# Optimization experiments

Measured on AMD Instinct MI355X. Metric: run time of the kernel, lower is better.

## Reference

```python
import jax, jax.numpy as jnp
import numpy as np

T, B, Y, X, C = 9, 2, 128, 128, 64
W = (T - 1) // 2
WIN, HEADS = 8, 4
EPS = 1e-3  # keras LayerNormalization default epsilon


def _get_indices(center, size):
    right = list(range(center, size, 2))
    left = list(range(center - 2, -1, -2))
    idx = np.array(left[::-1] + right, dtype=np.int32)
    return np.clip(idx, 1, size - 2)


def _pyramid_indices(t):
    levels = []
    size, center = t, (t - 1) // 2
    while size > 1:
        c = _get_indices(center, size)
        levels.append((c - 1, c, c + 1))
        center = int(np.where(c == center)[0][0])
        size = len(c)
    return levels


LEVELS = _pyramid_indices(T)            # 3 levels for T=9: sizes 5, 3, 1
CIN = [C * (l + 1) for l in range(len(LEVELS))]    # 64, 128, 192
COUT = [C * (l + 2) for l in range(len(LEVELS))]   # 128, 192, 256


def _window_attention(q, kv, wqkv, bqkv, wo, bo):
    # WindowSpatialAttention: non-overlapping WINxWIN windows, MHA of q over kv.
    N, Yd, Xd, Cd = q.shape
    w, h = WIN, HEADS
    dh = Cd // h
    nY, nX = Yd // w, Xd // w

    def to_win(t):
        t = t.reshape(N, nY, w, nX, w, Cd).transpose(0, 1, 3, 2, 4, 5)
        return t.reshape(N * nY * nX, w * w, Cd)

    qw, kvw = to_win(q), to_win(kv)
    qp = (qw @ wqkv[0] + bqkv[0]).reshape(-1, w * w, h, dh)
    kp = (kvw @ wqkv[1] + bqkv[1]).reshape(-1, w * w, h, dh)
    vp = (kvw @ wqkv[2] + bqkv[2]).reshape(-1, w * w, h, dh)
    logits = jnp.einsum('nqhd,nkhd->nhqk', qp, kp) / jnp.sqrt(jnp.float32(dh))
    attn = jax.nn.softmax(logits, axis=-1)
    out = jnp.einsum('nhqk,nkhd->nqhd', attn, vp).reshape(-1, w * w, Cd)
    out = out @ wo + bo
    out = out.reshape(N, nY, nX, w, w, Cd).transpose(0, 1, 3, 2, 4, 5)
    return out.reshape(N, Yd, Xd, Cd)


def _forward(x, params):
    fidx = np.arange(T) - W  # relative frame indices, static (non frame-aware)
    current = x
    level1 = None
    for l, (pi, ci, ni) in enumerate(LEVELS):
        emb, lng, lnb, wqkv, bqkv, wo, bo, cw, cb = params[l]
        cin = current.shape[-1]
        # additive relative temporal embedding, indexed by frame offset + W
        t_emb = emb[fidx + W]                       # [Tl, cin]
        cur = current + t_emb[:, None, None, None, :]
        mu = cur.mean(-1, keepdims=True)
        var = cur.var(-1, keepdims=True)
        cur = (cur - mu) * jax.lax.rsqrt(var + EPS) * lng + lnb
        S = len(ci)
        prev = cur[pi].reshape(S * B, Y, X, cin)
        cen = cur[ci].reshape(S * B, Y, X, cin)
        nxt = cur[ni].reshape(S * B, Y, X, cin)
        q = jnp.concatenate([cen, prev, cen, nxt], axis=0)
        kv = jnp.concatenate([prev, cen, nxt, cen], axis=0)
        att = _window_attention(q, kv, wqkv, bqkv, wo, bo)
        parts = jnp.split(att, 4, axis=0)           # SplitBatch(n_splits=4)
        comb = jnp.concatenate(parts, axis=-1)      # Combine: concat + 1x1 conv
        down = jax.nn.relu(comb @ cw + cb)
        if S > 1:
            down = down.reshape(S, B, Y, X, down.shape[-1])
        if l == 0:
            level1 = down
        current = down
        fidx = fidx[ci]
    return current, level1


def setup_inputs() -> dict:
    key = jax.random.key(0)
    ks = iter(jax.random.split(key, 64))
    inp = {'x': jax.random.normal(next(ks), (T, B, Y, X, C), jnp.float32)}
    for l, (ci, co) in enumerate(zip(CIN, COUT)):
        inp[f'emb{l}'] = 0.02 * jax.random.normal(next(ks), (T, ci), jnp.float32)
        inp[f'lng{l}'] = jnp.ones((ci,), jnp.float32)
        inp[f'lnb{l}'] = jnp.zeros((ci,), jnp.float32)
        inp[f'wqkv{l}'] = 0.02 * jax.random.normal(next(ks), (3, ci, ci), jnp.float32)
        inp[f'bqkv{l}'] = jnp.zeros((3, ci), jnp.float32)
        inp[f'wo{l}'] = 0.02 * jax.random.normal(next(ks), (ci, ci), jnp.float32)
        inp[f'bo{l}'] = jnp.zeros((ci,), jnp.float32)
        inp[f'cw{l}'] = 0.02 * jax.random.normal(next(ks), (4 * ci, co), jnp.float32)
        inp[f'cb{l}'] = jnp.zeros((co,), jnp.float32)
    return inp


def reference(x, emb0, lng0, lnb0, wqkv0, bqkv0, wo0, bo0, cw0, cb0,
              emb1, lng1, lnb1, wqkv1, bqkv1, wo1, bo1, cw1, cb1,
              emb2, lng2, lnb2, wqkv2, bqkv2, wo2, bo2, cw2, cb2):
    params = [
        (emb0, lng0, lnb0, wqkv0, bqkv0, wo0, bo0, cw0, cb0),
        (emb1, lng1, lnb1, wqkv1, bqkv1, wo1, bo1, cw1, cb1),
        (emb2, lng2, lnb2, wqkv2, bqkv2, wo2, bo2, cw2, cb2),
    ]
    return _forward(x, params)
```

## Files before the change

kernel.cpp:

```cpp
#include <hip/hip_runtime.h>

typedef _Float16 f16;
typedef f16 f16x4 __attribute__((ext_vector_type(4)));
typedef f16 f16x8 __attribute__((ext_vector_type(8)));
typedef float f32x4 __attribute__((ext_vector_type(4)));

#define MFMA16(a, b, c) __builtin_amdgcn_mfma_f32_16x16x16f16((a), (b), (c), 0, 0, 0)
#define MFMA32(a, b, c) __builtin_amdgcn_mfma_f32_16x16x32_f16((a), (b), (c), 0, 0, 0)

struct Meta   { int pi[5], ci[5], ni[5]; };
struct EmbMap { int m[9]; };

template <int CIN>
__global__ __launch_bounds__(256) void ln_kernel(
    const float* in, long lda, const float* __restrict__ emb,
    const float* __restrict__ lng, const float* __restrict__ lnb,
    f16* out, long ldo, EmbMap em) {
  long row = (long)blockIdx.x * 4 + (threadIdx.x >> 6);
  int t = (int)(row >> 15);
  int lane = threadIdx.x & 63;
  constexpr int NCH = CIN / 64;
  const float* xr = in + row * lda;
  const float* er = emb + (long)em.m[t] * CIN;
  float v[NCH];
  float s = 0.f;
#pragma unroll
  for (int i = 0; i < NCH; ++i) { int c = lane + (i << 6); v[i] = xr[c] + er[c]; s += v[i]; }
#pragma unroll
  for (int o = 32; o >= 1; o >>= 1) s += __shfl_xor(s, o);
  float mu = s * (1.f / CIN), ss = 0.f;
#pragma unroll
  for (int i = 0; i < NCH; ++i) { float d = v[i] - mu; ss += d * d; }
#pragma unroll
  for (int o = 32; o >= 1; o >>= 1) ss += __shfl_xor(ss, o);
  float inv = rsqrtf(ss * (1.f / CIN) + 1e-3f);
  f16* orow = out + row * ldo;
#pragma unroll
  for (int i = 0; i < NCH; ++i) {
    int c = lane + (i << 6);
    orow[c] = (f16)((v[i] - mu) * inv * lng[c] + lnb[c]);
  }
}

template <int CIN>
__global__ __launch_bounds__(64) void wT_kernel(const float* __restrict__ wqkv,
                                                f16* __restrict__ wqkvT) {
  int j = blockIdx.x;
  int which = j / CIN, jj = j % CIN;
  const float* src = wqkv + (long)which * CIN * CIN + jj;
  f16* dst = wqkvT + (long)j * CIN;
  for (int c = threadIdx.x; c < CIN; c += 64) dst[c] = (f16)src[(long)c * CIN];
}

template <int CIN, int CO>
__global__ __launch_bounds__(256) void woc_kernel(
    const float* __restrict__ wo, const float* __restrict__ bo,
    const float* __restrict__ cw, const float* __restrict__ cb,
    f16* __restrict__ wocT, float* __restrict__ fb) {
  __shared__ float scw[4 * CIN];
  __shared__ float red[256];
  int o = blockIdx.x;
  for (int i = threadIdx.x; i < 4 * CIN; i += 256) scw[i] = cw[(long)i * CO + o];
  __syncthreads();
  for (int pm = threadIdx.x; pm < 4 * CIN; pm += 256) {
    int p = pm / CIN, mm = pm % CIN;
    const float* wr = wo + (long)mm * CIN;
    const float* sc = scw + p * CIN;
    float s = 0.f;
    for (int c = 0; c < CIN; ++c) s += wr[c] * sc[c];
    wocT[(long)o * 4 * CIN + pm] = (f16)s;
  }
  float part = 0.f;
  for (int i = threadIdx.x; i < 4 * CIN; i += 256) part += bo[i % CIN] * scw[i];
  red[threadIdx.x] = part;
  __syncthreads();
  for (int st = 128; st > 0; st >>= 1) {
    if (threadIdx.x < st) red[threadIdx.x] += red[threadIdx.x + st];
    __syncthreads();
  }
  if (threadIdx.x == 0) fb[o] = cb[o] + red[0];
}

template <int CIN>
__global__ __launch_bounds__(256) void proj_kernel(
    const f16* __restrict__ cur, long lda, const f16* __restrict__ wT,
    const float* __restrict__ bqkv, f16* __restrict__ gq, f16* __restrict__ gk,
    f16* __restrict__ gvt) {
  constexpr int KS = CIN / 32;
  constexpr int NT = CIN / 16;
  constexpr int C8 = CIN / 8;
  __shared__ f16 sB[CIN * CIN];
  int which = blockIdx.x;
  long win = blockIdx.y;
  long img = win >> 8;
  int wid = (int)(win & 255);
  int wy = wid >> 4, wx = wid & 15;
  int w = threadIdx.x >> 6, lane = threadIdx.x & 63;
  int r16 = lane & 15, kq = lane >> 4;

  int tok = w * 16 + r16;
  long orig = img * 16384 + (long)(wy * 8 + (tok >> 3)) * 128 + wx * 8 + (tok & 7);
  const f16* arow = cur + orig * lda + kq * 8;
  f16x8 a[KS];
#pragma unroll
  for (int ks = 0; ks < KS; ++ks) a[ks] = *(const f16x8*)(arow + ks * 32);

  const f16* wsrc = wT + (long)which * CIN * CIN;
  for (int idx = threadIdx.x; idx < CIN * C8; idx += 256) {
    int j = idx / C8, c8 = idx % C8;
    f16x8 v = *(const f16x8*)(wsrc + idx * 8);
    int off = ((j * CIN + c8 * 8) * 2) ^ ((j & 7) << 4);
    *(f16x8*)((char*)sB + off) = v;
  }
  __syncthreads();

  f32x4 acc[NT] = {};
#pragma unroll
  for (int ks = 0; ks < KS; ++ks) {
#pragma unroll
    for (int t = 0; t < NT; ++t) {
      int off = (((t * 16 + r16) * CIN + ks * 32 + kq * 8) * 2) ^ ((r16 & 7) << 4);
      f16x8 bb = *(const f16x8*)((char*)sB + off);
      acc[t] = MFMA32(a[ks], bb, acc[t]);
    }
  }
  __syncthreads();

  if (which < 2) {
#pragma unroll
    for (int t = 0; t < NT; ++t) {
      float bias = bqkv[which * CIN + t * 16 + r16];
#pragma unroll
      for (int rg = 0; rg < 4; ++rg) {
        int r = w * 16 + kq * 4 + rg;
        int c = t * 16 + r16;
        int off = ((r * CIN + c) * 2) ^ ((r & 7) << 4);
        *(f16*)((char*)sB + off) = (f16)(acc[t][rg] + bias);
      }
    }
    __syncthreads();
    f16* dst = (which ? gk : gq) + win * 64 * CIN;
    for (int idx = threadIdx.x; idx < 64 * C8; idx += 256) {
      int r = idx / C8, c8 = idx % C8;
      int off = ((r * CIN + c8 * 8) * 2) ^ ((r & 7) << 4);
      f16x8 v = *(const f16x8*)((char*)sB + off);
      *(f16x8*)(dst + r * CIN + c8 * 8) = v;
    }
  } else {
#pragma unroll
    for (int t = 0; t < NT; ++t) {
      float bias = bqkv[2 * CIN + t * 16 + r16];
#pragma unroll
      for (int rg = 0; rg < 4; ++rg) {
        int c = t * 16 + r16;
        int pos = w * 16 + kq * 4 + rg;
        int off = ((c * 64 + pos) * 2) ^ ((c & 7) << 4);
        *(f16*)((char*)sB + off) = (f16)(acc[t][rg] + bias);
      }
    }
    __syncthreads();
    for (int c = threadIdx.x; c < CIN; c += 256) {
      f16* dst = gvt + (win * CIN + c) * 64;
#pragma unroll
      for (int p8 = 0; p8 < 8; ++p8) {
        int off = ((c * 64 + p8 * 8) * 2) ^ ((c & 7) << 4);
        *(f16x8*)(dst + p8 * 8) = *(const f16x8*)((char*)sB + off);
      }
    }
  }
}

template <int CIN, int DH, int CO>
__global__ __launch_bounds__(256) void attn_kernel(
    const f16* __restrict__ gq, const f16* __restrict__ gk,
    const f16* __restrict__ gvt, const f16* __restrict__ wocT,
    const float* __restrict__ fb, float* __restrict__ out, Meta m) {
  constexpr int NKS = DH / 16;
  constexpr int CO4 = CO / 4;
  constexpr int NTC = CO4 / 16;
  constexpr int NKD = CIN / 16;
  constexpr float scale = (DH == 16) ? 0.25f : (DH == 32) ? 0.1767766952966369f
                                                          : 0.1443375672974064f;
  __shared__ f16 O[64 * CIN];

  int img = blockIdx.y;
  int sidx = img >> 1, b = img & 1;
  int wid = blockIdx.x;
  int wy = wid >> 4, wx = wid & 15;
  int h = threadIdx.x >> 6, lane = threadIdx.x & 63;
  int r16 = lane & 15, kq = lane >> 4;
  int fpi = m.pi[sidx], fci = m.ci[sidx], fni = m.ni[sidx];

  f32x4 dn[NTC][4] = {};

  for (int p = 0; p < 4; ++p) {
    int qfr = (p == 1) ? fpi : ((p == 3) ? fni : fci);
    int kfr = (p == 0) ? fpi : ((p == 2) ? fni : fci);
    long qwin = (long)((qfr * 2 + b) * 256 + wid);
    long kwin = (long)((kfr * 2 + b) * 256 + wid);

    f16x4 kf[4][NKS];
#pragma unroll
    for (int tj = 0; tj < 4; ++tj)
#pragma unroll
      for (int ks = 0; ks < NKS; ++ks)
        kf[tj][ks] = *(const f16x4*)(gk + (kwin * 64 + tj * 16 + r16) * CIN +
                                     h * DH + ks * 16 + kq * 4);
    f32x4 sc[4][4] = {};
#pragma unroll
    for (int ti = 0; ti < 4; ++ti) {
      f16x4 qf[NKS];
#pragma unroll
      for (int ks = 0; ks < NKS; ++ks)
        qf[ks] = *(const f16x4*)(gq + (qwin * 64 + ti * 16 + r16) * CIN +
                                 h * DH + ks * 16 + kq * 4);
#pragma unroll
      for (int tj = 0; tj < 4; ++tj)
#pragma unroll
        for (int ks = 0; ks < NKS; ++ks)
          sc[tj][ti] = MFMA16(kf[tj][ks], qf[ks], sc[tj][ti]);
    }

    f16x4 pa[4][4];
#pragma unroll
    for (int ti = 0; ti < 4; ++ti) {
      float mx = -1e30f;
#pragma unroll
      for (int tj = 0; tj < 4; ++tj)
#pragma unroll
        for (int rg = 0; rg < 4; ++rg) mx = fmaxf(mx, sc[tj][ti][rg]);
      mx = fmaxf(mx, __shfl_xor(mx, 16));
      mx = fmaxf(mx, __shfl_xor(mx, 32));
      float sum = 0.f;
#pragma unroll
      for (int tj = 0; tj < 4; ++tj)
#pragma unroll
        for (int rg = 0; rg < 4; ++rg) {
          float e = __expf((sc[tj][ti][rg] - mx) * scale);
          sc[tj][ti][rg] = e;
          sum += e;
        }
      sum += __shfl_xor(sum, 16);
      sum += __shfl_xor(sum, 32);
      float inv = 1.f / sum;
#pragma unroll
      for (int tj = 0; tj < 4; ++tj) {
        f16x4 pv;
#pragma unroll
        for (int rg = 0; rg < 4; ++rg) pv[rg] = (f16)(sc[tj][ti][rg] * inv);
        pa[tj][ti] = pv;
      }
    }

#pragma unroll
    for (int dt = 0; dt < NKS; ++dt) {
      f16x4 va[4];
#pragma unroll
      for (int jt = 0; jt < 4; ++jt)
        va[jt] = *(const f16x4*)(gvt + (kwin * CIN + h * DH + dt * 16 + r16) * 64 +
                                 jt * 16 + kq * 4);
#pragma unroll
      for (int ti = 0; ti < 4; ++ti) {
        f32x4 po = {};
#pragma unroll
        for (int jt = 0; jt < 4; ++jt) po = MFMA16(va[jt], pa[jt][ti], po);
        int i = ti * 16 + r16;
        int c0 = h * DH + dt * 16 + kq * 4;
        f16x4 pk;
#pragma unroll
        for (int rg = 0; rg < 4; ++rg) pk[rg] = (f16)po[rg];
        int off = ((i * CIN + c0) * 2) ^ ((i & 7) << 4);
        *(f16x4*)((char*)O + off) = pk;
      }
    }
    __syncthreads();

#pragma unroll
    for (int ck = 0; ck < NKD; ++ck) {
      f16x4 ob[4];
#pragma unroll
      for (int ti = 0; ti < 4; ++ti) {
        int i = ti * 16 + r16;
        int off = ((i * CIN + ck * 16 + kq * 4) * 2) ^ ((i & 7) << 4);
        ob[ti] = *(const f16x4*)((char*)O + off);
      }
#pragma unroll
      for (int ot = 0; ot < NTC; ++ot) {
        f16x4 wa = *(const f16x4*)(wocT + ((long)(h * CO4 + ot * 16 + r16)) * 4 * CIN +
                                   p * CIN + ck * 16 + kq * 4);
#pragma unroll
        for (int ti = 0; ti < 4; ++ti) dn[ot][ti] = MFMA16(wa, ob[ti], dn[ot][ti]);
      }
    }
    __syncthreads();
  }

#pragma unroll
  for (int ot = 0; ot < NTC; ++ot) {
    f32x4 fb4 = *(const f32x4*)(fb + h * CO4 + ot * 16 + kq * 4);
#pragma unroll
    for (int ti = 0; ti < 4; ++ti) {
      int i = ti * 16 + r16;
      long gtok = (long)img * 16384 + (wy * 8 + (i >> 3)) * 128 + wx * 8 + (i & 7);
      f32x4 v;
#pragma unroll
      for (int rg = 0; rg < 4; ++rg) v[rg] = fmaxf(dn[ot][ti][rg] + fb4[rg], 0.f);
      *(f32x4*)(out + gtok * CO + h * CO4 + ot * 16 + kq * 4) = v;
    }
  }
}

extern "C" void kernel_launch(void* const* d_in, const int* in_sizes, int n_in,
                              void* d_out, int out_size, void* d_ws, size_t ws_size,
                              hipStream_t stream) {
  const float* x = (const float*)d_in[0];
#define PRM(l, k) ((const float*)d_in[1 + 9 * (l) + (k)])
  float* outCur = (float*)d_out;
  float* outL1 = (float*)d_out + 8388608;

  char* ws = (char*)d_ws;
  const size_t OFF_B = 125829120ull;
  const size_t OFF_W = OFF_B + 75497472ull;
  f16* qkvbase = (f16*)ws;
  char* wsB = ws + OFF_B;
  float* accum1 = (float*)wsB;
  f16* wqkvT = (f16*)(ws + OFF_W);
  f16* wocT = (f16*)(ws + OFF_W + 262144);
  float* fb = (float*)(ws + OFF_W + 262144 + 524288);

  Meta m0 = {{0, 1, 3, 5, 6}, {1, 2, 4, 6, 7}, {2, 3, 5, 7, 8}};
  Meta m1 = {{0, 1, 2, 0, 0}, {1, 2, 3, 0, 0}, {2, 3, 4, 0, 0}};
  Meta m2 = {{0, 0, 0, 0, 0}, {1, 0, 0, 0, 0}, {2, 0, 0, 0, 0}};
  EmbMap em0 = {{0, 1, 2, 3, 4, 5, 6, 7, 8}};
  EmbMap em1 = {{1, 2, 4, 6, 7, 0, 0, 0, 0}};
  EmbMap em2 = {{2, 4, 6, 0, 0, 0, 0, 0, 0}};

  {
    constexpr int CIN = 64, DH = 16, CO = 128, TL = 9, S = 5;
    long ntok = (long)TL * 2 * 16384;
    f16 *gq = qkvbase, *gk = gq + ntok * CIN, *gvt = gk + ntok * CIN;
    f16* cur = (f16*)wsB;
    ln_kernel<CIN><<<dim3((unsigned)(ntok / 4)), 256, 0, stream>>>(
        x, CIN, PRM(0, 0), PRM(0, 1), PRM(0, 2), cur, CIN, em0);
    wT_kernel<CIN><<<dim3(3 * CIN), 64, 0, stream>>>(PRM(0, 3), wqkvT);
    woc_kernel<CIN, CO><<<dim3(CO), 256, 0, stream>>>(PRM(0, 5), PRM(0, 6), PRM(0, 7), PRM(0, 8), wocT, fb);
    proj_kernel<CIN><<<dim3(3, (unsigned)(ntok / 64)), 256, 0, stream>>>(
        cur, CIN, wqkvT, PRM(0, 4), gq, gk, gvt);
    attn_kernel<CIN, DH, CO><<<dim3(256, S * 2), 256, 0, stream>>>(
        gq, gk, gvt, wocT, fb, outL1, m0);
  }
  {
    constexpr int CIN = 128, DH = 32, CO = 192, TL = 5, S = 3;
    long ntok = (long)TL * 2 * 16384;
    f16 *gq = qkvbase, *gk = gq + ntok * CIN, *gvt = gk + ntok * CIN;
    f16* cur = (f16*)wsB;
    ln_kernel<CIN><<<dim3((unsigned)(ntok / 4)), 256, 0, stream>>>(
        outL1, CIN, PRM(1, 0), PRM(1, 1), PRM(1, 2), cur, CIN, em1);
    wT_kernel<CIN><<<dim3(3 * CIN), 64, 0, stream>>>(PRM(1, 3), wqkvT);
    woc_kernel<CIN, CO><<<dim3(CO), 256, 0, stream>>>(PRM(1, 5), PRM(1, 6), PRM(1, 7), PRM(1, 8), wocT, fb);
    proj_kernel<CIN><<<dim3(3, (unsigned)(ntok / 64)), 256, 0, stream>>>(
        cur, CIN, wqkvT, PRM(1, 4), gq, gk, gvt);
    attn_kernel<CIN, DH, CO><<<dim3(256, S * 2), 256, 0, stream>>>(
        gq, gk, gvt, wocT, fb, accum1, m1);
  }
  {
    constexpr int CIN = 192, DH = 48, CO = 256, TL = 3, S = 1;
    long ntok = (long)TL * 2 * 16384;
    f16 *gq = qkvbase, *gk = gq + ntok * CIN, *gvt = gk + ntok * CIN;
    f16* cur = (f16*)accum1;
    ln_kernel<CIN><<<dim3((unsigned)(ntok / 4)), 256, 0, stream>>>(
        accum1, CIN, PRM(2, 0), PRM(2, 1), PRM(2, 2), cur, 384, em2);
    wT_kernel<CIN><<<dim3(3 * CIN), 64, 0, stream>>>(PRM(2, 3), wqkvT);
    woc_kernel<CIN, CO><<<dim3(CO), 256, 0, stream>>>(PRM(2, 5), PRM(2, 6), PRM(2, 7), PRM(2, 8), wocT, fb);
    proj_kernel<CIN><<<dim3(3, (unsigned)(ntok / 64)), 256, 0, stream>>>(
        cur, 384, wqkvT, PRM(2, 4), gq, gk, gvt);
    attn_kernel<CIN, DH, CO><<<dim3(256, S * 2), 256, 0, stream>>>(
        gq, gk, gvt, wocT, fb, outCur, m2);
  }
#undef PRM
}
```

Before: 690.8 us.

## Use 16x16x32 MFMA, drop softmax max pass, double-buffer attention LDS tile

The attention kernel now uses the 16x16x32 f16 MFMA for the QK^T product and for the fused output/conv projection. To feed it, the fused projection weights are repacked into an 8-element interleaved layout. Softmax drops the row-max subtraction and computes exp2 with a pre-folded log2e scale. V fragments are loaded before the score computation, and the shared O tile is double-buffered so one __syncthreads per pass can be removed. Skipping the max subtraction risks overflow if logits become large, and the fully unrolled pass loop may increase register pressure.

```diff
diff --git a/kernel.cpp b/kernel.cpp
--- a/kernel.cpp
+++ b/kernel.cpp
@@ -56,7 +56,7 @@
 __global__ __launch_bounds__(256) void woc_kernel(
     const float* __restrict__ wo, const float* __restrict__ bo,
     const float* __restrict__ cw, const float* __restrict__ cb,
-    f16* __restrict__ wocT, float* __restrict__ fb) {
+    f16* __restrict__ wocA, float* __restrict__ fb) {
   __shared__ float scw[4 * CIN];
   __shared__ float red[256];
   int o = blockIdx.x;
@@ -68,7 +68,7 @@
     const float* sc = scw + p * CIN;
     float s = 0.f;
     for (int c = 0; c < CIN; ++c) s += wr[c] * sc[c];
-    wocT[(long)o * 4 * CIN + pm] = (f16)s;
+    wocA[((long)(pm >> 3) * CO + o) * 8 + (pm & 7)] = (f16)s;
   }
   float part = 0.f;
   for (int i = threadIdx.x; i < 4 * CIN; i += 256) part += bo[i % CIN] * scw[i];
@@ -173,15 +173,18 @@
 template <int CIN, int DH, int CO>
 __global__ __launch_bounds__(256) void attn_kernel(
     const f16* __restrict__ gq, const f16* __restrict__ gk,
-    const f16* __restrict__ gvt, const f16* __restrict__ wocT,
+    const f16* __restrict__ gvt, const f16* __restrict__ wocA,
     const float* __restrict__ fb, float* __restrict__ out, Meta m) {
   constexpr int NKS = DH / 16;
+  constexpr int NK8 = DH / 32;
+  constexpr int NK4 = (DH % 32) / 16;
   constexpr int CO4 = CO / 4;
   constexpr int NTC = CO4 / 16;
-  constexpr int NKD = CIN / 16;
+  constexpr int NKD = CIN / 32;
   constexpr float scale = (DH == 16) ? 0.25f : (DH == 32) ? 0.1767766952966369f
                                                           : 0.1443375672974064f;
-  __shared__ f16 O[64 * CIN];
+  constexpr float escale = scale * 1.4426950408889634f;
+  __shared__ f16 O[2][64 * CIN];
 
   int img = blockIdx.y;
   int sidx = img >> 1, b = img & 1;
@@ -193,51 +196,66 @@
 
   f32x4 dn[NTC][4] = {};
 
+#pragma unroll
   for (int p = 0; p < 4; ++p) {
     int qfr = (p == 1) ? fpi : ((p == 3) ? fni : fci);
     int kfr = (p == 0) ? fpi : ((p == 2) ? fni : fci);
     long qwin = (long)((qfr * 2 + b) * 256 + wid);
     long kwin = (long)((kfr * 2 + b) * 256 + wid);
 
-    f16x4 kf[4][NKS];
-#pragma unroll
-    for (int tj = 0; tj < 4; ++tj)
-#pragma unroll
-      for (int ks = 0; ks < NKS; ++ks)
-        kf[tj][ks] = *(const f16x4*)(gk + (kwin * 64 + tj * 16 + r16) * CIN +
-                                     h * DH + ks * 16 + kq * 4);
-    f32x4 sc[4][4] = {};
+    f16x8 kf8[4][NK8 ? NK8 : 1];
+    f16x4 kf4[4][NK4 ? NK4 : 1];
+#pragma unroll
+    for (int tj = 0; tj < 4; ++tj) {
+      const f16* kb = gk + (kwin * 64 + tj * 16 + r16) * CIN + h * DH;
+      if constexpr (NK8 > 0)
+#pragma unroll
+        for (int n = 0; n < NK8; ++n)
+          kf8[tj][n] = *(const f16x8*)(kb + n * 32 + kq * 8);
+      if constexpr (NK4 > 0)
+#pragma unroll
+        for (int n = 0; n < NK4; ++n)
+          kf4[tj][n] = *(const f16x4*)(kb + NK8 * 32 + n * 16 + kq * 4);
+    }
+    f16x4 va[NKS][4];
+#pragma unroll
+    for (int dt = 0; dt < NKS; ++dt)
+#pragma unroll
+      for (int jt = 0; jt < 4; ++jt)
+        va[dt][jt] = *(const f16x4*)(gvt + (kwin * CIN + h * DH + dt * 16 + r16) * 64 +
+                                     jt * 16 + kq * 4);
+
+    f16x4 pa[4][4];
 #pragma unroll
     for (int ti = 0; ti < 4; ++ti) {
-      f16x4 qf[NKS];
-#pragma unroll
-      for (int ks = 0; ks < NKS; ++ks)
-        qf[ks] = *(const f16x4*)(gq + (qwin * 64 + ti * 16 + r16) * CIN +
-                                 h * DH + ks * 16 + kq * 4);
+      const f16* qb = gq + (qwin * 64 + ti * 16 + r16) * CIN + h * DH;
+      f32x4 s4[4] = {};
+      if constexpr (NK8 > 0) {
+        f16x8 qf8[NK8];
+#pragma unroll
+        for (int n = 0; n < NK8; ++n) qf8[n] = *(const f16x8*)(qb + n * 32 + kq * 8);
+#pragma unroll
+        for (int tj = 0; tj < 4; ++tj)
+#pragma unroll
+          for (int n = 0; n < NK8; ++n) s4[tj] = MFMA32(kf8[tj][n], qf8[n], s4[tj]);
+      }
+      if constexpr (NK4 > 0) {
+        f16x4 qf4[NK4];
+#pragma unroll
+        for (int n = 0; n < NK4; ++n)
+          qf4[n] = *(const f16x4*)(qb + NK8 * 32 + n * 16 + kq * 4);
+#pragma unroll
+        for (int tj = 0; tj < 4; ++tj)
+#pragma unroll
+          for (int n = 0; n < NK4; ++n) s4[tj] = MFMA16(kf4[tj][n], qf4[n], s4[tj]);
+      }
+      float sum = 0.f;
 #pragma unroll
       for (int tj = 0; tj < 4; ++tj)
 #pragma unroll
-        for (int ks = 0; ks < NKS; ++ks)
-          sc[tj][ti] = MFMA16(kf[tj][ks], qf[ks], sc[tj][ti]);
-    }
-
-    f16x4 pa[4][4];
-#pragma unroll
-    for (int ti = 0; ti < 4; ++ti) {
-      float mx = -1e30f;
-#pragma unroll
-      for (int tj = 0; tj < 4; ++tj)
-#pragma unroll
-        for (int rg = 0; rg < 4; ++rg) mx = fmaxf(mx, sc[tj][ti][rg]);
-      mx = fmaxf(mx, __shfl_xor(mx, 16));
-      mx = fmaxf(mx, __shfl_xor(mx, 32));
-      float sum = 0.f;
-#pragma unroll
-      for (int tj = 0; tj < 4; ++tj)
-#pragma unroll
         for (int rg = 0; rg < 4; ++rg) {
-          float e = __expf((sc[tj][ti][rg] - mx) * scale);
-          sc[tj][ti][rg] = e;
+          float e = __builtin_amdgcn_exp2f(s4[tj][rg] * escale);
+          s4[tj][rg] = e;
           sum += e;
         }
       sum += __shfl_xor(sum, 16);
@@ -247,52 +265,47 @@
       for (int tj = 0; tj < 4; ++tj) {
         f16x4 pv;
 #pragma unroll
-        for (int rg = 0; rg < 4; ++rg) pv[rg] = (f16)(sc[tj][ti][rg] * inv);
+        for (int rg = 0; rg < 4; ++rg) pv[rg] = (f16)(s4[tj][rg] * inv);
         pa[tj][ti] = pv;
       }
     }
 
+    char* Ob = (char*)O[p & 1];
 #pragma unroll
     for (int dt = 0; dt < NKS; ++dt) {
-      f16x4 va[4];
-#pragma unroll
-      for (int jt = 0; jt < 4; ++jt)
-        va[jt] = *(const f16x4*)(gvt + (kwin * CIN + h * DH + dt * 16 + r16) * 64 +
-                                 jt * 16 + kq * 4);
 #pragma unroll
       for (int ti = 0; ti < 4; ++ti) {
         f32x4 po = {};
 #pragma unroll
-        for (int jt = 0; jt < 4; ++jt) po = MFMA16(va[jt], pa[jt][ti], po);
+        for (int jt = 0; jt < 4; ++jt) po = MFMA16(va[dt][jt], pa[jt][ti], po);
         int i = ti * 16 + r16;
         int c0 = h * DH + dt * 16 + kq * 4;
         f16x4 pk;
 #pragma unroll
         for (int rg = 0; rg < 4; ++rg) pk[rg] = (f16)po[rg];
         int off = ((i * CIN + c0) * 2) ^ ((i & 7) << 4);
-        *(f16x4*)((char*)O + off) = pk;
+        *(f16x4*)(Ob + off) = pk;
       }
     }
     __syncthreads();
 
 #pragma unroll
     for (int ck = 0; ck < NKD; ++ck) {
-      f16x4 ob[4];
+      f16x8 ob[4];
 #pragma unroll
       for (int ti = 0; ti < 4; ++ti) {
         int i = ti * 16 + r16;
-        int off = ((i * CIN + ck * 16 + kq * 4) * 2) ^ ((i & 7) << 4);
-        ob[ti] = *(const f16x4*)((char*)O + off);
-      }
+        int off = ((i * CIN + ck * 32 + kq * 8) * 2) ^ ((i & 7) << 4);
+        ob[ti] = *(const f16x8*)(Ob + off);
+      }
+      long pm = (long)(p * CIN + ck * 32 + kq * 8);
 #pragma unroll
       for (int ot = 0; ot < NTC; ++ot) {
-        f16x4 wa = *(const f16x4*)(wocT + ((long)(h * CO4 + ot * 16 + r16)) * 4 * CIN +
-                                   p * CIN + ck * 16 + kq * 4);
-#pragma unroll
-        for (int ti = 0; ti < 4; ++ti) dn[ot][ti] = MFMA16(wa, ob[ti], dn[ot][ti]);
-      }
-    }
-    __syncthreads();
+        f16x8 wa = *(const f16x8*)(wocA + ((pm >> 3) * CO + h * CO4 + ot * 16 + r16) * 8);
+#pragma unroll
+        for (int ti = 0; ti < 4; ++ti) dn[ot][ti] = MFMA32(wa, ob[ti], dn[ot][ti]);
+      }
+    }
   }
 
 #pragma unroll
@@ -325,7 +338,7 @@
   char* wsB = ws + OFF_B;
   float* accum1 = (float*)wsB;
   f16* wqkvT = (f16*)(ws + OFF_W);
-  f16* wocT = (f16*)(ws + OFF_W + 262144);
+  f16* wocA = (f16*)(ws + OFF_W + 262144);
   float* fb = (float*)(ws + OFF_W + 262144 + 524288);
 
   Meta m0 = {{0, 1, 3, 5, 6}, {1, 2, 4, 6, 7}, {2, 3, 5, 7, 8}};
@@ -343,11 +356,11 @@
     ln_kernel<CIN><<<dim3((unsigned)(ntok / 4)), 256, 0, stream>>>(
         x, CIN, PRM(0, 0), PRM(0, 1), PRM(0, 2), cur, CIN, em0);
     wT_kernel<CIN><<<dim3(3 * CIN), 64, 0, stream>>>(PRM(0, 3), wqkvT);
-    woc_kernel<CIN, CO><<<dim3(CO), 256, 0, stream>>>(PRM(0, 5), PRM(0, 6), PRM(0, 7), PRM(0, 8), wocT, fb);
+    woc_kernel<CIN, CO><<<dim3(CO), 256, 0, stream>>>(PRM(0, 5), PRM(0, 6), PRM(0, 7), PRM(0, 8), wocA, fb);
     proj_kernel<CIN><<<dim3(3, (unsigned)(ntok / 64)), 256, 0, stream>>>(
         cur, CIN, wqkvT, PRM(0, 4), gq, gk, gvt);
     attn_kernel<CIN, DH, CO><<<dim3(256, S * 2), 256, 0, stream>>>(
-        gq, gk, gvt, wocT, fb, outL1, m0);
+        gq, gk, gvt, wocA, fb, outL1, m0);
   }
   {
     constexpr int CIN = 128, DH = 32, CO = 192, TL = 5, S = 3;
@@ -357,11 +370,11 @@
     ln_kernel<CIN><<<dim3((unsigned)(ntok / 4)), 256, 0, stream>>>(
         outL1, CIN, PRM(1, 0), PRM(1, 1), PRM(1, 2), cur, CIN, em1);
     wT_kernel<CIN><<<dim3(3 * CIN), 64, 0, stream>>>(PRM(1, 3), wqkvT);
-    woc_kernel<CIN, CO><<<dim3(CO), 256, 0, stream>>>(PRM(1, 5), PRM(1, 6), PRM(1, 7), PRM(1, 8), wocT, fb);
+    woc_kernel<CIN, CO><<<dim3(CO), 256, 0, stream>>>(PRM(1, 5), PRM(1, 6), PRM(1, 7), PRM(1, 8), wocA, fb);
     proj_kernel<CIN><<<dim3(3, (unsigned)(ntok / 64)), 256, 0, stream>>>(
         cur, CIN, wqkvT, PRM(1, 4), gq, gk, gvt);
     attn_kernel<CIN, DH, CO><<<dim3(256, S * 2), 256, 0, stream>>>(
-        gq, gk, gvt, wocT, fb, accum1, m1);
+        gq, gk, gvt, wocA, fb, accum1, m1);
   }
   {
     constexpr int CIN = 192, DH = 48, CO = 256, TL = 3, S = 1;
@@ -371,11 +384,11 @@
     ln_kernel<CIN><<<dim3((unsigned)(ntok / 4)), 256, 0, stream>>>(
         accum1, CIN, PRM(2, 0), PRM(2, 1), PRM(2, 2), cur, 384, em2);
     wT_kernel<CIN><<<dim3(3 * CIN), 64, 0, stream>>>(PRM(2, 3), wqkvT);
-    woc_kernel<CIN, CO><<<dim3(CO), 256, 0, stream>>>(PRM(2, 5), PRM(2, 6), PRM(2, 7), PRM(2, 8), wocT, fb);
+    woc_kernel<CIN, CO><<<dim3(CO), 256, 0, stream>>>(PRM(2, 5), PRM(2, 6), PRM(2, 7), PRM(2, 8), wocA, fb);
     proj_kernel<CIN><<<dim3(3, (unsigned)(ntok / 64)), 256, 0, stream>>>(
         cur, 384, wqkvT, PRM(2, 4), gq, gk, gvt);
     attn_kernel<CIN, DH, CO><<<dim3(256, S * 2), 256, 0, stream>>>(
-        gq, gk, gvt, wocT, fb, outCur, m2);
+        gq, gk, gvt, wocA, fb, outCur, m2);
   }
 #undef PRM
 }
```

Measured after the change: 629.8 us. 8.8% less time.
